# Kernel tuning notes

Hardware: AMD Instinct MI355X
Metric: run time of the kernel (lower is better)

## Reference

```python
import jax, jax.numpy as jnp
import numpy as np

VOCAB = 50000          # max binary columnId
N_NUM = 5000           # numerical feature ids = 1..5000
N_CAT = VOCAB + 1 - N_NUM  # categorical table rows (incl. padding row 0)
D = 128
B, L = 512, 512


def setup_inputs() -> dict:
    key = jax.random.key(0)
    k1, k2, k3, k4, k5 = jax.random.split(key, 5)
    feature_ids = jax.random.randint(k1, (B, L), 0, VOCAB + 1)
    feature_values = jax.random.normal(k2, (B, L), dtype=jnp.float32)
    cat_table = jax.random.normal(k3, (N_CAT, D), dtype=jnp.float32) * 0.02
    cat_table = cat_table.at[0].set(0.0)  # padding_idx=0
    num_weight = jax.random.normal(k4, (N_NUM, D), dtype=jnp.float32) * 0.02
    num_bias = jax.random.normal(k5, (N_NUM, D), dtype=jnp.float32) * 0.02
    # lookup buffers, exactly as built in __init__ with numerical ids = 1..N_NUM
    input_to_numeric = np.zeros(VOCAB + 1, dtype=np.int64)
    num_ids = np.arange(1, N_NUM + 1)
    input_to_numeric[num_ids] = np.arange(1, N_NUM + 1)
    input_to_categorical = np.zeros(VOCAB + 1, dtype=np.int64)
    cat_ids = np.where(input_to_numeric == 0)[0]
    input_to_categorical[cat_ids[1:]] = np.arange(1, cat_ids.size)
    return {
        "feature_ids": feature_ids,
        "feature_values": feature_values,
        "cat_table": cat_table,
        "num_weight": num_weight,
        "num_bias": num_bias,
        "input_to_numeric": jnp.asarray(input_to_numeric),
        "input_to_categorical": jnp.asarray(input_to_categorical),
    }


def reference(feature_ids, feature_values, cat_table, num_weight, num_bias,
              input_to_numeric, input_to_categorical):
    # numerical mask: isin(feature_ids, numerical_feature_ids) == nonzero mapped idx
    n_idx = input_to_numeric[feature_ids]                 # [B,L], 1..N_NUM or 0
    numerical_mask = n_idx > 0                            # [B,L]
    # numerical path: weight[id] * value + bias[id]  (1-based mapped -> 0-based row)
    n_row = jnp.maximum(n_idx - 1, 0)                     # [B,L]
    num_emb = num_weight[n_row] * feature_values[..., None] + num_bias[n_row]  # [B,L,D]
    # categorical path: route numerical positions to padding id 0
    cat_features = jnp.where(numerical_mask, 0, feature_ids)
    c_idx = input_to_categorical[cat_features]            # [B,L]
    cat_emb = cat_table[c_idx]                            # [B,L,D]
    # merge
    return jnp.where(numerical_mask[..., None], num_emb, cat_emb)
```

## Files before the change

kernel.cpp:

```cpp
#include <hip/hip_runtime.h>


constexpr int D  = 128;
constexpr int BL = 512 * 512;

typedef float vfloat4 __attribute__((ext_vector_type(4)));

union F4 {
    float4  h;
    vfloat4 n;
};

__global__ __launch_bounds__(256) void emb_kernel(
    const int*    __restrict__ feature_ids,
    const float*  __restrict__ feature_values,
    const float*  __restrict__ cat_table,
    const float*  __restrict__ num_weight,
    const float*  __restrict__ num_bias,
    float*        __restrict__ out)
{
    const int tid = threadIdx.x;
    const long long gbase = (long long)blockIdx.x * 1024;

    int   id[4];
    float v[4];
    int   pos[4], sub[4];
#pragma unroll
    for (int pass = 0; pass < 4; ++pass) {
        const long long g = gbase + pass * 256 + tid;
        pos[pass] = (int)(g >> 5);
        sub[pass] = (int)(g & 31);
        id[pass]  = feature_ids[pos[pass]];
        v[pass]   = feature_values[pos[pass]];
    }

    F4 r[4];
#pragma unroll
    for (int pass = 0; pass < 4; ++pass) {
        const int i = id[pass];
        if (i >= 1 && i <= 5000) {
            const long long off = (long long)(i - 1) * D + sub[pass] * 4;
            const float4 w = *(const float4*)(num_weight + off);
            const float4 b = *(const float4*)(num_bias   + off);
            const float  x = v[pass];
            r[pass].h.x = fmaf(w.x, x, b.x);
            r[pass].h.y = fmaf(w.y, x, b.y);
            r[pass].h.z = fmaf(w.z, x, b.z);
            r[pass].h.w = fmaf(w.w, x, b.w);
        } else {
            const int c = (i > 5000) ? (i - 5000) : 0;
            r[pass].h = *(const float4*)(cat_table + (long long)c * D + sub[pass] * 4);
        }
    }

#pragma unroll
    for (int pass = 0; pass < 4; ++pass) {
        vfloat4* dst = (vfloat4*)(out + (long long)pos[pass] * D + sub[pass] * 4);
        __builtin_nontemporal_store(r[pass].n, dst);
    }
}

extern "C" void kernel_launch(void* const* d_in, const int* in_sizes, int n_in,
                              void* d_out, int out_size, void* d_ws, size_t ws_size,
                              hipStream_t stream) {
    const int*   feature_ids    = (const int*)  d_in[0];
    const float* feature_values = (const float*)d_in[1];
    const float* cat_table      = (const float*)d_in[2];
    const float* num_weight     = (const float*)d_in[3];
    const float* num_bias       = (const float*)d_in[4];
    float*       out            = (float*)      d_out;

    const int blocks = (BL * 32) / 1024;
    emb_kernel<<<blocks, 256, 0, stream>>>(
        feature_ids, feature_values, cat_table, num_weight, num_bias, out);
}
```

Measured before the change: 183.4 us.

## Remap work per wave with shuffled ids and branchless gather-FMA

Each wave now handles 16 positions. Each lane loads one id and value, and lanes share them with __shfl, so every lane no longer reloads the id per pass. The numeric and categorical paths are merged into a single branchless weight*scale+bias load pair. The categorical case uses row 0 of cat_table as a zero bias, which relies on the padding row being zero. Each thread now keeps 8 row-fragment loads in flight instead of 4, to raise memory-level parallelism. The cost is an extra (cached) load for categorical rows and more registers.

```diff
diff --git a/kernel.cpp b/kernel.cpp
--- a/kernel.cpp
+++ b/kernel.cpp
@@ -3,13 +3,12 @@
 
 constexpr int D  = 128;
 constexpr int BL = 512 * 512;
+constexpr int POS_PER_WAVE  = 16;
+constexpr int WAVES_PER_BLK = 4;
+constexpr int POS_PER_BLK   = POS_PER_WAVE * WAVES_PER_BLK;
 
 typedef float vfloat4 __attribute__((ext_vector_type(4)));
-
-union F4 {
-    float4  h;
-    vfloat4 n;
-};
+union F4 { float4 h; vfloat4 n; };
 
 __global__ __launch_bounds__(256) void emb_kernel(
     const int*    __restrict__ feature_ids,
@@ -19,44 +18,45 @@
     const float*  __restrict__ num_bias,
     float*        __restrict__ out)
 {
-    const int tid = threadIdx.x;
-    const long long gbase = (long long)blockIdx.x * 1024;
+    const int tid  = threadIdx.x;
+    const int lane = tid & 63;
+    const int wave = tid >> 6;
+    const int wbase = blockIdx.x * POS_PER_BLK + wave * POS_PER_WAVE;
 
-    int   id[4];
-    float v[4];
-    int   pos[4], sub[4];
+    const int  myp = lane & 15;
+    const int  id  = feature_ids[wbase + myp];
+    const float mv = feature_values[wbase + myp];
+    const int route = (id >= 1 && id <= 5000) ? -id
+                    : ((id > 5000) ? id - 5000 : 0);
+
+    float4 av[8], bv[8];
+    float  sc[8];
 #pragma unroll
-    for (int pass = 0; pass < 4; ++pass) {
-        const long long g = gbase + pass * 256 + tid;
-        pos[pass] = (int)(g >> 5);
-        sub[pass] = (int)(g & 31);
-        id[pass]  = feature_ids[pos[pass]];
-        v[pass]   = feature_values[pos[pass]];
+    for (int k = 0; k < 8; ++k) {
+        const int p  = k * 2 + (lane >> 5);
+        const int rt = __shfl(route, p);
+        const float vv = __shfl(mv, p);
+        const bool isnum = rt < 0;
+        const long long rowoff = isnum ? (long long)(-rt - 1) * D
+                                       : (long long)rt * D;
+        const float* a = isnum ? (num_weight + rowoff) : (cat_table + rowoff);
+        const float* b = isnum ? (num_bias   + rowoff) : cat_table;
+        sc[k] = isnum ? vv : 1.0f;
+        const int sub = (lane & 31) * 4;
+        av[k] = *(const float4*)(a + sub);
+        bv[k] = *(const float4*)(b + sub);
     }
 
-    F4 r[4];
+    float* const obase = out + (long long)wbase * D;
 #pragma unroll
-    for (int pass = 0; pass < 4; ++pass) {
-        const int i = id[pass];
-        if (i >= 1 && i <= 5000) {
-            const long long off = (long long)(i - 1) * D + sub[pass] * 4;
-            const float4 w = *(const float4*)(num_weight + off);
-            const float4 b = *(const float4*)(num_bias   + off);
-            const float  x = v[pass];
-            r[pass].h.x = fmaf(w.x, x, b.x);
-            r[pass].h.y = fmaf(w.y, x, b.y);
-            r[pass].h.z = fmaf(w.z, x, b.z);
-            r[pass].h.w = fmaf(w.w, x, b.w);
-        } else {
-            const int c = (i > 5000) ? (i - 5000) : 0;
-            r[pass].h = *(const float4*)(cat_table + (long long)c * D + sub[pass] * 4);
-        }
-    }
-
-#pragma unroll
-    for (int pass = 0; pass < 4; ++pass) {
-        vfloat4* dst = (vfloat4*)(out + (long long)pos[pass] * D + sub[pass] * 4);
-        __builtin_nontemporal_store(r[pass].n, dst);
+    for (int k = 0; k < 8; ++k) {
+        F4 r;
+        r.h.x = fmaf(av[k].x, sc[k], bv[k].x);
+        r.h.y = fmaf(av[k].y, sc[k], bv[k].y);
+        r.h.z = fmaf(av[k].z, sc[k], bv[k].z);
+        r.h.w = fmaf(av[k].w, sc[k], bv[k].w);
+        vfloat4* dst = (vfloat4*)(obase + (k * 64 + lane) * 4);
+        __builtin_nontemporal_store(r.n, dst);
     }
 }
 
@@ -70,7 +70,7 @@
     const float* num_bias       = (const float*)d_in[4];
     float*       out            = (float*)      d_out;
 
-    const int blocks = (BL * 32) / 1024;
+    const int blocks = BL / POS_PER_BLK;
     emb_kernel<<<blocks, 256, 0, stream>>>(
         feature_ids, feature_values, cat_table, num_weight, num_bias, out);
 }
```

Measured after the change: 183.4 us. About the same (-0.0%).
